# Performance work log

Hardware: AMD Instinct MI355X
Metric: run time of the kernel (lower is better)

Reference implementation:

```python
import jax, jax.numpy as jnp
import numpy as np

N, E, F_IN, NUM_GRAPHS, K = 50000, 500000, 160, 128, 3


def _glorot(k, shape):
    lim = np.sqrt(6.0 / (shape[-2] + shape[-1])).astype(np.float32)
    return jax.random.uniform(k, shape, jnp.float32, -lim, lim)


def setup_inputs() -> dict:
    key = jax.random.key(0)
    ks = jax.random.split(key, 8)
    x = jax.random.normal(ks[0], (N, F_IN), jnp.float32)
    edge_index = jax.random.randint(ks[1], (2, E), 0, N)
    edge_attr = jax.random.uniform(ks[2], (E,), jnp.float32)
    batch = jnp.sort(jax.random.randint(ks[3], (N,), 0, NUM_GRAPHS))
    W1 = _glorot(ks[4], (K, F_IN, 128)); b1 = jnp.zeros((128,), jnp.float32)
    W2 = _glorot(ks[5], (K, 128, 64)); b2 = jnp.zeros((64,), jnp.float32)
    W3 = _glorot(ks[6], (K, 64, 32)); b3 = jnp.zeros((32,), jnp.float32)
    Wl = _glorot(ks[7], (32, 2)); bl = jnp.zeros((2,), jnp.float32)
    return dict(x=x, edge_index=edge_index, edge_attr=edge_attr, batch=batch,
                W1=W1, b1=b1, W2=W2, b2=b2, W3=W3, b3=b3, Wl=Wl, bl=bl)


def _cheb_norm(src, dst, edge_attr, n):
    # PyG ChebConv: sym-normalized Laplacian, lambda_max=2 =>
    # L_hat = (2/lmax)*L_sym - I = -D^{-1/2} A D^{-1/2} (diagonal = 0)
    deg = jax.ops.segment_sum(edge_attr, src, num_segments=n)
    safe = jnp.where(deg > 0, deg, 1.0)
    dinv = jnp.where(deg > 0, jax.lax.rsqrt(safe), 0.0)
    return -dinv[src] * edge_attr * dinv[dst]


def _propagate(x, src, dst, w, n):
    # out[dst] += w * x[src]  (sparse L_hat @ x)
    return jax.ops.segment_sum(w[:, None] * x[src], dst, num_segments=n)


def _cheb_conv(x, src, dst, w, W, b, n):
    # Chebyshev recurrence: T0 = x, T1 = L_hat x, Tk = 2 L_hat T(k-1) - T(k-2)
    tx0 = x
    out = tx0 @ W[0]
    tx1 = _propagate(tx0, src, dst, w, n)
    out = out + tx1 @ W[1]
    for k in range(2, W.shape[0]):
        tx2 = 2.0 * _propagate(tx1, src, dst, w, n) - tx0
        out = out + tx2 @ W[k]
        tx0, tx1 = tx1, tx2
    return out + b


def reference(x, edge_index, edge_attr, batch, W1, b1, W2, b2, W3, b3, Wl, bl):
    n = x.shape[0]
    src, dst = edge_index[0], edge_index[1]
    w = _cheb_norm(src, dst, edge_attr, n)
    h = jax.nn.relu(_cheb_conv(x, src, dst, w, W1, b1, n))
    h = jax.nn.relu(_cheb_conv(h, src, dst, w, W2, b2, n))
    h = jax.nn.relu(_cheb_conv(h, src, dst, w, W3, b3, n))
    # global_mean_pool over graph ids (dropout omitted: eval mode)
    sums = jax.ops.segment_sum(h, batch, num_segments=NUM_GRAPHS)
    cnt = jax.ops.segment_sum(jnp.ones((n,), h.dtype), batch, num_segments=NUM_GRAPHS)
    pooled = sums / jnp.maximum(cnt, 1.0)[:, None]
    return pooled @ Wl + bl
```

## Files before the change

kernel.cpp:

```cpp
#include <hip/hip_runtime.h>

#define N_NODES 50000
#define N_EDGES 500000
#define NUM_G   128
#define SCAN_NB 49
#define PN      (SCAN_NB * 1024)
#define NCX     64
#define ECH     7813
#define RNG     8192
#define NRY     7
#define HVB     (2 * NCX * NRY)
#define CONVB   7813
#define WPREPB  360

typedef __attribute__((ext_vector_type(8))) short short8;
typedef __attribute__((ext_vector_type(4))) float f32x4;

__device__ __forceinline__ unsigned f2bf(float x) {
    unsigned u = __float_as_uint(x);
    return (u + 0x7FFFu + ((u >> 16) & 1u)) >> 16;
}
__device__ __forceinline__ float bf2f(unsigned h) {
    return __uint_as_float(h << 16);
}

__device__ __forceinline__ void wprep_one(const float* __restrict__ W, unsigned short* __restrict__ WT,
                                          int t, int FIN, int F) {
    int n = t / FIN, k = t - n * FIN;
    int sel = n / F, c = n - sel * F;
    float v;
    if (sel == 0) v = W[(size_t)k * F + c] - W[(size_t)2 * FIN * F + (size_t)k * F + c];
    else          v = W[(size_t)sel * FIN * F + (size_t)k * F + c];
    WT[t] = (unsigned short)f2bf(v);
}

__global__ __launch_bounds__(256)
void prep_kernel(const int* __restrict__ src, const int* __restrict__ dst,
                 const float* __restrict__ ea,
                 float* __restrict__ pdeg, int* __restrict__ pcnt,
                 const float* __restrict__ x, unsigned short* __restrict__ Xb,
                 const float* __restrict__ W1, const float* __restrict__ W2,
                 const float* __restrict__ W3,
                 unsigned short* __restrict__ WT1, unsigned short* __restrict__ WT2,
                 unsigned short* __restrict__ WT3) {
    __shared__ unsigned lh[RNG];
    int vb = blockIdx.x, tid = threadIdx.x;
    if (vb < HVB) {
        bool isdeg = vb < NCX * NRY;
        int v2 = isdeg ? vb : vb - NCX * NRY;
        int xk = v2 & 63, y = v2 >> 6;
        int base = y * RNG;
        for (int i = tid; i < RNG; i += 256) lh[i] = 0u;
        __syncthreads();
        int e0 = xk * ECH, e1 = min(e0 + ECH, N_EDGES);
        if (isdeg) {
            for (int e = e0 + tid; e < e1; e += 256) {
                int s = src[e];
                if ((unsigned)(s - base) < RNG) atomicAdd((float*)&lh[s - base], ea[e]);
            }
        } else {
            for (int e = e0 + tid; e < e1; e += 256) {
                int d = dst[e];
                if ((unsigned)(d - base) < RNG) atomicAdd((int*)&lh[d - base], 1);
            }
        }
        __syncthreads();
        if (isdeg) {
            for (int i = tid; i < RNG; i += 256) {
                int n = base + i;
                if (n < PN) pdeg[(size_t)xk * PN + n] = ((float*)lh)[i];
            }
        } else {
            for (int i = tid; i < RNG; i += 256) {
                int n = base + i;
                if (n < PN) pcnt[(size_t)xk * PN + n] = ((int*)lh)[i];
            }
        }
    } else if (vb < HVB + CONVB) {
        int t = (vb - HVB) * 256 + tid;
        if (t < N_NODES * 160 / 4) {
            float4 v = reinterpret_cast<const float4*>(x)[t];
            ushort4 r;
            r.x = (unsigned short)f2bf(v.x);
            r.y = (unsigned short)f2bf(v.y);
            r.z = (unsigned short)f2bf(v.z);
            r.w = (unsigned short)f2bf(v.w);
            *reinterpret_cast<ushort4*>(Xb + (size_t)t * 4) = r;
        }
    } else {
        int t = (vb - HVB - CONVB) * 256 + tid;
        if (t < 61440)      wprep_one(W1, WT1, t, 160, 128);
        else if (t < 86016) wprep_one(W2, WT2, t - 61440, 128, 64);
        else if (t < 92160) wprep_one(W3, WT3, t - 86016, 64, 32);
    }
}

__global__ __launch_bounds__(256)
void reduce_scan_kernel(const float* __restrict__ pdeg, int* __restrict__ pcnt,
                        float* __restrict__ dinv, int* __restrict__ cnt,
                        int* __restrict__ partial) {
    int b = blockIdx.x, t = threadIdx.x;
    int i0 = b * 1024 + t * 4;
    float d0 = 0.f, d1 = 0.f, d2 = 0.f, d3 = 0.f;
    int r0 = 0, r1 = 0, r2 = 0, r3 = 0;
    for (int x = 0; x < NCX; ++x) {
        float4 pv = *reinterpret_cast<const float4*>(pdeg + (size_t)x * PN + i0);
        int4   cv = *reinterpret_cast<const int4*>(pcnt + (size_t)x * PN + i0);
        *reinterpret_cast<int4*>(pcnt + (size_t)x * PN + i0) = make_int4(r0, r1, r2, r3);
        d0 += pv.x; d1 += pv.y; d2 += pv.z; d3 += pv.w;
        r0 += cv.x; r1 += cv.y; r2 += cv.z; r3 += cv.w;
    }
    float dd[4] = {d0, d1, d2, d3};
    int   rr[4] = {r0, r1, r2, r3};
    int s = 0;
    #pragma unroll
    for (int j = 0; j < 4; ++j) {
        int n = i0 + j;
        if (n < N_NODES) {
            float dv = dd[j], r = 0.f;
            if (dv > 0.f) {
                r = rsqrtf(dv);
                r = r * (1.5f - 0.5f * dv * r * r);
            }
            dinv[n] = r;
            cnt[n] = rr[j];
            s += rr[j];
        } else {
            cnt[n] = 0;
        }
    }
    __shared__ int red[256];
    red[t] = s;
    __syncthreads();
    for (int off = 128; off > 0; off >>= 1) {
        if (t < off) red[t] += red[t + off];
        __syncthreads();
    }
    if (t == 0) partial[b] = red[0];
}

__global__ void scan_offsets_kernel(int* __restrict__ partial, int* __restrict__ rowptr,
                                    int nb, int n) {
    int t = threadIdx.x;
    int orig = (t < nb) ? partial[t] : 0;
    int v = orig;
    for (int off = 1; off < 64; off <<= 1) {
        int u = __shfl_up(v, off, 64);
        if (t >= off) v += u;
    }
    if (t < nb) partial[t] = v - orig;
    if (t == nb - 1) rowptr[n] = v;
}

__global__ void scan_final_kernel(const int* __restrict__ cnt, const int* __restrict__ partial,
                                  int* __restrict__ rowptr, int n) {
    int b = blockIdx.x, t = threadIdx.x;
    int4 v = reinterpret_cast<const int4*>(cnt)[b * 256 + t];
    int s = v.x + v.y + v.z + v.w;
    __shared__ int red[256];
    red[t] = s;
    __syncthreads();
    for (int off = 1; off < 256; off <<= 1) {
        int u = (t >= off) ? red[t - off] : 0;
        __syncthreads();
        red[t] += u;
        __syncthreads();
    }
    int excl = partial[b] + ((t == 0) ? 0 : red[t - 1]);
    int i0 = b * 1024 + t * 4;
    if (i0 < n)     rowptr[i0]     = excl;
    if (i0 + 1 < n) rowptr[i0 + 1] = excl + v.x;
    if (i0 + 2 < n) rowptr[i0 + 2] = excl + v.x + v.y;
    if (i0 + 3 < n) rowptr[i0 + 3] = excl + v.x + v.y + v.z;
}

__global__ __launch_bounds__(256)
void scatter_kernel(const int* __restrict__ src, const int* __restrict__ dst,
                    const float* __restrict__ ea,
                    const int* __restrict__ rowptr, const int* __restrict__ pcnt,
                    int2* __restrict__ csr) {
    __shared__ int cursor[RNG];
    int x = blockIdx.x, y = blockIdx.y, tid = threadIdx.x;
    int base = y * RNG;
    for (int i = tid; i < RNG; i += 256) {
        int n = base + i;
        cursor[i] = (n < N_NODES) ? (rowptr[n] + pcnt[(size_t)x * PN + n]) : 0;
    }
    __syncthreads();
    int e0 = x * ECH, e1 = min(e0 + ECH, N_EDGES);
    for (int e = e0 + tid; e < e1; e += 256) {
        int d = dst[e];
        if ((unsigned)(d - base) < RNG) {
            int pos = atomicAdd(&cursor[d - base], 1);
            int2 ew;
            ew.x = src[e];
            ew.y = __float_as_int(ea[e]);
            csr[pos] = ew;
        }
    }
}

template<int FIN, int F>
__launch_bounds__(256)
__global__ void cheb_gemm(const unsigned short* __restrict__ Xb, const unsigned short* __restrict__ WT,
                          const float* __restrict__ dinv,
                          unsigned short* __restrict__ Y0, unsigned short* __restrict__ Y1,
                          unsigned short* __restrict__ Y2,
                          int nrows) {
    constexpr int KT = FIN / 32;
    constexpr int NT = F / 32;
    constexpr int SA = FIN + 8;
    constexpr int F8 = FIN / 8;
    __shared__ short Bs[32 * SA];

    int tid = threadIdx.x;
    int lane = tid & 63, w = tid >> 6;
    int m0 = blockIdx.x * 64;
    int g = blockIdx.y;
    unsigned short* Ys = (g == 0) ? Y0 : (g == 1) ? Y1 : Y2;

    int colb = lane & 15;
    int q8 = (lane >> 4) << 3;
    int rq = (lane >> 4) << 2;
    int arow = m0 + w * 16 + colb;
    bool rok = arow < nrows;

    short8 afr[KT];
    #pragma unroll
    for (int kt = 0; kt < KT; ++kt) {
        short8 z = {0, 0, 0, 0, 0, 0, 0, 0};
        afr[kt] = rok ? *reinterpret_cast<const short8*>(Xb + (size_t)arow * FIN + (kt << 5) + q8) : z;
    }

    for (int nt = 0; nt < NT; ++nt) {
        int n0 = (g * NT + nt) << 5;
        __syncthreads();
        for (int span = tid; span < 32 * F8; span += 256) {
            int r = span / F8, c8 = (span - r * F8) << 3;
            int pr = (r < 16) ? (r << 1) : (((r - 16) << 1) + 1);
            *reinterpret_cast<uint4*>(&Bs[r * SA + c8]) =
                *reinterpret_cast<const uint4*>(WT + (size_t)(n0 + pr) * FIN + c8);
        }
        __syncthreads();

        f32x4 acc0 = {0.f, 0.f, 0.f, 0.f}, acc1 = acc0;
        #pragma unroll
        for (int kt = 0; kt < KT; ++kt) {
            short8 b0 = *reinterpret_cast<const short8*>(&Bs[colb * SA + (kt << 5) + q8]);
            short8 b1 = *reinterpret_cast<const short8*>(&Bs[(colb + 16) * SA + (kt << 5) + q8]);
            acc0 = __builtin_amdgcn_mfma_f32_16x16x32_bf16(afr[kt], b0, acc0, 0, 0, 0);
            acc1 = __builtin_amdgcn_mfma_f32_16x16x32_bf16(afr[kt], b1, acc1, 0, 0, 0);
        }

        int lc = (nt << 5) + (colb << 1);
        #pragma unroll
        for (int r = 0; r < 4; ++r) {
            int orow = m0 + w * 16 + rq + r;
            if (orow < nrows) {
                float sc = (g == 2) ? dinv[orow] : 1.0f;
                unsigned pack = f2bf(acc0[r] * sc) | (f2bf(acc1[r] * sc) << 16);
                *reinterpret_cast<unsigned*>(Ys + (size_t)orow * F + lc) = pack;
            }
        }
    }
}

__device__ __forceinline__ void acc8(float* acc, uint4 p, float wv) {
    acc[0] += wv * bf2f(p.x & 0xFFFFu);
    acc[1] += wv * __uint_as_float(p.x & 0xFFFF0000u);
    acc[2] += wv * bf2f(p.y & 0xFFFFu);
    acc[3] += wv * __uint_as_float(p.y & 0xFFFF0000u);
    acc[4] += wv * bf2f(p.z & 0xFFFFu);
    acc[5] += wv * __uint_as_float(p.z & 0xFFFF0000u);
    acc[6] += wv * bf2f(p.w & 0xFFFFu);
    acc[7] += wv * __uint_as_float(p.w & 0xFFFF0000u);
}

__device__ __forceinline__ void expand8(uint4 p, float* o) {
    o[0] = bf2f(p.x & 0xFFFFu);
    o[1] = __uint_as_float(p.x & 0xFFFF0000u);
    o[2] = bf2f(p.y & 0xFFFFu);
    o[3] = __uint_as_float(p.y & 0xFFFF0000u);
    o[4] = bf2f(p.z & 0xFFFFu);
    o[5] = __uint_as_float(p.z & 0xFFFF0000u);
    o[6] = bf2f(p.w & 0xFFFFu);
    o[7] = __uint_as_float(p.w & 0xFFFF0000u);
}

template<int F, int MODE>
__launch_bounds__(256)
__global__ void gather_kernel(const unsigned short* __restrict__ X, const int2* __restrict__ csr,
                              const int* __restrict__ rowptr, const float* __restrict__ dinv,
                              const unsigned short* __restrict__ Y, const float* __restrict__ bias,
                              unsigned short* __restrict__ O, int n) {
    constexpr int FQ8 = F >> 3;
    constexpr int DPB = 256 / FQ8;
    constexpr int CAP = 2048;
    __shared__ int2 scsr[CAP];
    __shared__ int srp[DPB + 1];
    int tid = threadIdx.x;
    int db0 = blockIdx.x * DPB;
    if (tid <= DPB) srp[tid] = rowptr[min(db0 + tid, n)];
    __syncthreads();
    int ebeg = srp[0];
    int ecnt = srp[DPB] - ebeg;
    bool staged = ecnt <= CAP;
    if (staged) {
        for (int i = tid; i < ecnt; i += 256)
            scsr[i] = csr[ebeg + i];
    }
    __syncthreads();

    int d = db0 + tid / FQ8;
    if (d >= n) return;
    int f8 = (tid % FQ8) << 3;
    float acc[8] = {0.f, 0.f, 0.f, 0.f, 0.f, 0.f, 0.f, 0.f};

    if (staged) {
        int beg = srp[tid / FQ8] - ebeg, end = srp[tid / FQ8 + 1] - ebeg;
        int i = beg;
        for (; i + 7 < end; i += 8) {
            int2 e0 = scsr[i],     e1 = scsr[i + 1], e2 = scsr[i + 2], e3 = scsr[i + 3];
            int2 e4 = scsr[i + 4], e5 = scsr[i + 5], e6 = scsr[i + 6], e7 = scsr[i + 7];
            uint4 p0 = *reinterpret_cast<const uint4*>(X + (size_t)e0.x * F + f8);
            uint4 p1 = *reinterpret_cast<const uint4*>(X + (size_t)e1.x * F + f8);
            uint4 p2 = *reinterpret_cast<const uint4*>(X + (size_t)e2.x * F + f8);
            uint4 p3 = *reinterpret_cast<const uint4*>(X + (size_t)e3.x * F + f8);
            uint4 p4 = *reinterpret_cast<const uint4*>(X + (size_t)e4.x * F + f8);
            uint4 p5 = *reinterpret_cast<const uint4*>(X + (size_t)e5.x * F + f8);
            uint4 p6 = *reinterpret_cast<const uint4*>(X + (size_t)e6.x * F + f8);
            uint4 p7 = *reinterpret_cast<const uint4*>(X + (size_t)e7.x * F + f8);
            acc8(acc, p0, __int_as_float(e0.y));
            acc8(acc, p1, __int_as_float(e1.y));
            acc8(acc, p2, __int_as_float(e2.y));
            acc8(acc, p3, __int_as_float(e3.y));
            acc8(acc, p4, __int_as_float(e4.y));
            acc8(acc, p5, __int_as_float(e5.y));
            acc8(acc, p6, __int_as_float(e6.y));
            acc8(acc, p7, __int_as_float(e7.y));
        }
        for (; i + 3 < end; i += 4) {
            int2 e0 = scsr[i], e1 = scsr[i + 1], e2 = scsr[i + 2], e3 = scsr[i + 3];
            uint4 p0 = *reinterpret_cast<const uint4*>(X + (size_t)e0.x * F + f8);
            uint4 p1 = *reinterpret_cast<const uint4*>(X + (size_t)e1.x * F + f8);
            uint4 p2 = *reinterpret_cast<const uint4*>(X + (size_t)e2.x * F + f8);
            uint4 p3 = *reinterpret_cast<const uint4*>(X + (size_t)e3.x * F + f8);
            acc8(acc, p0, __int_as_float(e0.y));
            acc8(acc, p1, __int_as_float(e1.y));
            acc8(acc, p2, __int_as_float(e2.y));
            acc8(acc, p3, __int_as_float(e3.y));
        }
        for (; i < end; ++i) {
            int2 e = scsr[i];
            uint4 p = *reinterpret_cast<const uint4*>(X + (size_t)e.x * F + f8);
            acc8(acc, p, __int_as_float(e.y));
        }
    } else {
        int beg = srp[tid / FQ8], end = srp[tid / FQ8 + 1];
        for (int i = beg; i < end; ++i) {
            int2 e = csr[i];
            uint4 p = *reinterpret_cast<const uint4*>(X + (size_t)e.x * F + f8);
            acc8(acc, p, __int_as_float(e.y));
        }
    }

    float y[8];
    expand8(*reinterpret_cast<const uint4*>(Y + (size_t)d * F + f8), y);
    float dv = dinv[d];
    float v[8];
    if (MODE == 0) {
        float dv2 = 2.f * dv;
        #pragma unroll
        for (int j = 0; j < 8; ++j) v[j] = dv * (y[j] - dv2 * acc[j]);
    } else {
        float4 ba = *reinterpret_cast<const float4*>(bias + f8);
        float4 bb = *reinterpret_cast<const float4*>(bias + f8 + 4);
        v[0] = fmaxf(y[0] - dv * acc[0] + ba.x, 0.f);
        v[1] = fmaxf(y[1] - dv * acc[1] + ba.y, 0.f);
        v[2] = fmaxf(y[2] - dv * acc[2] + ba.z, 0.f);
        v[3] = fmaxf(y[3] - dv * acc[3] + ba.w, 0.f);
        v[4] = fmaxf(y[4] - dv * acc[4] + bb.x, 0.f);
        v[5] = fmaxf(y[5] - dv * acc[5] + bb.y, 0.f);
        v[6] = fmaxf(y[6] - dv * acc[6] + bb.z, 0.f);
        v[7] = fmaxf(y[7] - dv * acc[7] + bb.w, 0.f);
    }
    uint4 o;
    o.x = f2bf(v[0]) | (f2bf(v[1]) << 16);
    o.y = f2bf(v[2]) | (f2bf(v[3]) << 16);
    o.z = f2bf(v[4]) | (f2bf(v[5]) << 16);
    o.w = f2bf(v[6]) | (f2bf(v[7]) << 16);
    *reinterpret_cast<uint4*>(O + (size_t)d * F + f8) = o;
}

__device__ __forceinline__ int lower_bound_dev(const int* __restrict__ a, int n, int v) {
    int lo = 0, hi = n;
    while (lo < hi) {
        int mid = (lo + hi) >> 1;
        if (a[mid] < v) lo = mid + 1; else hi = mid;
    }
    return lo;
}

__global__ void pool_kernel(const unsigned short* __restrict__ H, const int* __restrict__ batch,
                            const float* __restrict__ Wl, const float* __restrict__ bl,
                            float* __restrict__ out, int n) {
    int g = blockIdx.x;
    int start = lower_bound_dev(batch, n, g);
    int end   = lower_bound_dev(batch, n, g + 1);
    int tid = threadIdx.x;
    int f = tid & 31;
    int sub = tid >> 5;
    float acc = 0.0f;
    for (int i = start + sub; i < end; i += 8)
        acc += bf2f((unsigned)H[(size_t)i * 32 + f]);
    __shared__ float red[256];
    red[tid] = acc;
    __syncthreads();
    if (tid < 128) red[tid] += red[tid + 128];
    __syncthreads();
    if (tid < 64) red[tid] += red[tid + 64];
    __syncthreads();
    if (tid < 32) red[tid] += red[tid + 32];
    __syncthreads();
    if (tid < 2) {
        int cnt = end - start;
        float inv = 1.0f / (float)(cnt > 0 ? cnt : 1);
        float o = bl[tid];
        for (int f2 = 0; f2 < 32; ++f2)
            o += red[f2] * inv * Wl[f2 * 2 + tid];
        out[g * 2 + tid] = o;
    }
}

extern "C" void kernel_launch(void* const* d_in, const int* in_sizes, int n_in,
                              void* d_out, int out_size, void* d_ws, size_t ws_size,
                              hipStream_t stream) {
    const float* x     = (const float*)d_in[0];
    const int*   ei    = (const int*)d_in[1];
    const float* ea    = (const float*)d_in[2];
    const int*   batch = (const int*)d_in[3];
    const float* W1 = (const float*)d_in[4];
    const float* b1 = (const float*)d_in[5];
    const float* W2 = (const float*)d_in[6];
    const float* b2 = (const float*)d_in[7];
    const float* W3 = (const float*)d_in[8];
    const float* b3 = (const float*)d_in[9];
    const float* Wl = (const float*)d_in[10];
    const float* bl = (const float*)d_in[11];
    float* out = (float*)d_out;
    char* ws = (char*)d_ws;

    const int* src = ei;
    const int* dst = ei + N_EDGES;

    size_t off = 0;
    auto alloc = [&](size_t bytes) { char* p = ws + off; off += (bytes + 255) & ~(size_t)255; return p; };
    float* pdeg    = (float*)alloc((size_t)NCX * PN * 4);
    int*   pcnt    = (int*)  alloc((size_t)NCX * PN * 4);
    float* dinv    = (float*)alloc(N_NODES * 4);
    int*   cnt     = (int*)  alloc((size_t)PN * 4);
    int*   partial = (int*)  alloc(SCAN_NB * 4);
    int*   rowptr  = (int*)  alloc((N_NODES + 1) * 4);
    int2*  csr     = (int2*) alloc((size_t)N_EDGES * 8);
    unsigned short* Xb  = (unsigned short*)alloc((size_t)N_NODES * 160 * 2);
    unsigned short* Y0  = (unsigned short*)alloc((size_t)N_NODES * 128 * 2);
    unsigned short* Y1  = (unsigned short*)alloc((size_t)N_NODES * 128 * 2);
    unsigned short* Y2  = (unsigned short*)alloc((size_t)N_NODES * 128 * 2);
    unsigned short* U   = (unsigned short*)alloc((size_t)N_NODES * 128 * 2);
    unsigned short* WT1 = (unsigned short*)alloc((size_t)384 * 160 * 2);
    unsigned short* WT2 = (unsigned short*)alloc((size_t)192 * 128 * 2);
    unsigned short* WT3 = (unsigned short*)alloc((size_t)96 * 64 * 2);

    const int BT = 256;

    prep_kernel<<<HVB + CONVB + WPREPB, BT, 0, stream>>>(src, dst, ea, pdeg, pcnt,
                                                         x, Xb, W1, W2, W3, WT1, WT2, WT3);
    reduce_scan_kernel<<<SCAN_NB, BT, 0, stream>>>(pdeg, pcnt, dinv, cnt, partial);
    scan_offsets_kernel<<<1, 64, 0, stream>>>(partial, rowptr, SCAN_NB, N_NODES);
    scan_final_kernel<<<SCAN_NB, BT, 0, stream>>>(cnt, partial, rowptr, N_NODES);
    scatter_kernel<<<dim3(NCX, NRY), BT, 0, stream>>>(src, dst, ea, rowptr, pcnt, csr);

    dim3 ggrid((N_NODES + 63) / 64, 3);
    auto gb = [&](int F) { int DPB = 256 / (F / 8); return (N_NODES + DPB - 1) / DPB; };

    cheb_gemm<160, 128><<<ggrid, BT, 0, stream>>>(Xb, WT1, dinv, Y0, Y1, Y2, N_NODES);
    gather_kernel<128, 0><<<gb(128), BT, 0, stream>>>(Y2, csr, rowptr, dinv, Y1, nullptr, U, N_NODES);
    gather_kernel<128, 1><<<gb(128), BT, 0, stream>>>(U, csr, rowptr, dinv, Y0, b1, Xb, N_NODES);

    cheb_gemm<128, 64><<<ggrid, BT, 0, stream>>>(Xb, WT2, dinv, Y0, Y1, Y2, N_NODES);
    gather_kernel<64, 0><<<gb(64), BT, 0, stream>>>(Y2, csr, rowptr, dinv, Y1, nullptr, U, N_NODES);
    gather_kernel<64, 1><<<gb(64), BT, 0, stream>>>(U, csr, rowptr, dinv, Y0, b2, Xb, N_NODES);

    cheb_gemm<64, 32><<<ggrid, BT, 0, stream>>>(Xb, WT3, dinv, Y0, Y1, Y2, N_NODES);
    gather_kernel<32, 0><<<gb(32), BT, 0, stream>>>(Y2, csr, rowptr, dinv, Y1, nullptr, U, N_NODES);
    gather_kernel<32, 1><<<gb(32), BT, 0, stream>>>(U, csr, rowptr, dinv, Y0, b3, Xb, N_NODES);

    pool_kernel<<<NUM_G, BT, 0, stream>>>(Xb, batch, Wl, bl, out, N_NODES);
}
```

Before: 322.3 us.

## Fuse scan offsets into scan_final and co-launch scatter with first GEMM

Folds the single-block scan_offsets kernel into scan_final_kernel, with each block recomputing the 49-entry prefix via wave shuffles. Merges the CSR scatter and the layer-1 Chebyshev GEMM into one launch that dispatches on block index, since they are independent and can overlap. This removes two kernel launches and the serialization between them. In exchange the merged kernel reserves 32KB of shared memory for all blocks, which may reduce occupancy for the GEMM blocks.

```diff
diff --git a/kernel.cpp b/kernel.cpp
--- a/kernel.cpp
+++ b/kernel.cpp
@@ -12,6 +12,8 @@
 #define HVB     (2 * NCX * NRY)
 #define CONVB   7813
 #define WPREPB  360
+#define SCVB    (NCX * NRY)
+#define GEMM_MB 782
 
 typedef __attribute__((ext_vector_type(8))) short short8;
 typedef __attribute__((ext_vector_type(4))) float f32x4;
@@ -139,25 +141,26 @@
     if (t == 0) partial[b] = red[0];
 }
 
-__global__ void scan_offsets_kernel(int* __restrict__ partial, int* __restrict__ rowptr,
-                                    int nb, int n) {
-    int t = threadIdx.x;
-    int orig = (t < nb) ? partial[t] : 0;
-    int v = orig;
-    for (int off = 1; off < 64; off <<= 1) {
-        int u = __shfl_up(v, off, 64);
-        if (t >= off) v += u;
-    }
-    if (t < nb) partial[t] = v - orig;
-    if (t == nb - 1) rowptr[n] = v;
-}
-
-__global__ void scan_final_kernel(const int* __restrict__ cnt, const int* __restrict__ partial,
-                                  int* __restrict__ rowptr, int n) {
+__global__ __launch_bounds__(256)
+void scan_final_kernel(const int* __restrict__ cnt, const int* __restrict__ partial,
+                       int* __restrict__ rowptr, int n) {
     int b = blockIdx.x, t = threadIdx.x;
+    __shared__ int red[256];
+    __shared__ int sh_off, sh_tot;
+    if (t < 64) {
+        int orig = (t < SCAN_NB) ? partial[t] : 0;
+        int v = orig;
+        #pragma unroll
+        for (int off = 1; off < 64; off <<= 1) {
+            int u = __shfl_up(v, off, 64);
+            if (t >= off) v += u;
+        }
+        if (t == b) sh_off = v - orig;
+        if (t == SCAN_NB - 1) sh_tot = v;
+    }
+    __syncthreads();
     int4 v = reinterpret_cast<const int4*>(cnt)[b * 256 + t];
     int s = v.x + v.y + v.z + v.w;
-    __shared__ int red[256];
     red[t] = s;
     __syncthreads();
     for (int off = 1; off < 256; off <<= 1) {
@@ -166,21 +169,22 @@
         red[t] += u;
         __syncthreads();
     }
-    int excl = partial[b] + ((t == 0) ? 0 : red[t - 1]);
+    int excl = sh_off + ((t == 0) ? 0 : red[t - 1]);
     int i0 = b * 1024 + t * 4;
     if (i0 < n)     rowptr[i0]     = excl;
     if (i0 + 1 < n) rowptr[i0 + 1] = excl + v.x;
     if (i0 + 2 < n) rowptr[i0 + 2] = excl + v.x + v.y;
     if (i0 + 3 < n) rowptr[i0 + 3] = excl + v.x + v.y + v.z;
-}
-
-__global__ __launch_bounds__(256)
-void scatter_kernel(const int* __restrict__ src, const int* __restrict__ dst,
-                    const float* __restrict__ ea,
-                    const int* __restrict__ rowptr, const int* __restrict__ pcnt,
-                    int2* __restrict__ csr) {
-    __shared__ int cursor[RNG];
-    int x = blockIdx.x, y = blockIdx.y, tid = threadIdx.x;
+    if (b == SCAN_NB - 1 && t == 0) rowptr[n] = sh_tot;
+}
+
+__device__ void scatter_body(int vb, const int* __restrict__ src, const int* __restrict__ dst,
+                             const float* __restrict__ ea,
+                             const int* __restrict__ rowptr, const int* __restrict__ pcnt,
+                             int2* __restrict__ csr, unsigned char* smraw) {
+    int* cursor = (int*)smraw;
+    int tid = threadIdx.x;
+    int x = vb & 63, y = vb >> 6;
     int base = y * RNG;
     for (int i = tid; i < RNG; i += 256) {
         int n = base + i;
@@ -201,22 +205,19 @@
 }
 
 template<int FIN, int F>
-__launch_bounds__(256)
-__global__ void cheb_gemm(const unsigned short* __restrict__ Xb, const unsigned short* __restrict__ WT,
-                          const float* __restrict__ dinv,
+__device__ void gemm_body(int bx, int g, const unsigned short* __restrict__ Xb,
+                          const unsigned short* __restrict__ WT, const float* __restrict__ dinv,
                           unsigned short* __restrict__ Y0, unsigned short* __restrict__ Y1,
-                          unsigned short* __restrict__ Y2,
-                          int nrows) {
+                          unsigned short* __restrict__ Y2, int nrows, unsigned char* smraw) {
     constexpr int KT = FIN / 32;
     constexpr int NT = F / 32;
     constexpr int SA = FIN + 8;
     constexpr int F8 = FIN / 8;
-    __shared__ short Bs[32 * SA];
+    short* Bs = (short*)smraw;
 
     int tid = threadIdx.x;
     int lane = tid & 63, w = tid >> 6;
-    int m0 = blockIdx.x * 64;
-    int g = blockIdx.y;
+    int m0 = bx * 64;
     unsigned short* Ys = (g == 0) ? Y0 : (g == 1) ? Y1 : Y2;
 
     int colb = lane & 15;
@@ -263,6 +264,35 @@
             }
         }
     }
+}
+
+__global__ __launch_bounds__(256)
+void sg_kernel(const int* __restrict__ src, const int* __restrict__ dst,
+               const float* __restrict__ ea,
+               const int* __restrict__ rowptr, const int* __restrict__ pcnt,
+               int2* __restrict__ csr,
+               const unsigned short* __restrict__ Xb, const unsigned short* __restrict__ WT1,
+               const float* __restrict__ dinv,
+               unsigned short* __restrict__ Y0, unsigned short* __restrict__ Y1,
+               unsigned short* __restrict__ Y2) {
+    __shared__ alignas(16) unsigned char sm[32768];
+    int vb = blockIdx.x;
+    if (vb < SCVB) {
+        scatter_body(vb, src, dst, ea, rowptr, pcnt, csr, sm);
+    } else {
+        int v2 = vb - SCVB;
+        gemm_body<160, 128>(v2 % GEMM_MB, v2 / GEMM_MB, Xb, WT1, dinv, Y0, Y1, Y2, N_NODES, sm);
+    }
+}
+
+template<int FIN, int F>
+__launch_bounds__(256)
+__global__ void cheb_gemm(const unsigned short* __restrict__ Xb, const unsigned short* __restrict__ WT,
+                          const float* __restrict__ dinv,
+                          unsigned short* __restrict__ Y0, unsigned short* __restrict__ Y1,
+                          unsigned short* __restrict__ Y2, int nrows) {
+    __shared__ alignas(16) unsigned char sm[32 * (FIN + 8) * 2];
+    gemm_body<FIN, F>(blockIdx.x, blockIdx.y, Xb, WT, dinv, Y0, Y1, Y2, nrows, sm);
 }
 
 __device__ __forceinline__ void acc8(float* acc, uint4 p, float wv) {
@@ -476,14 +506,13 @@
     prep_kernel<<<HVB + CONVB + WPREPB, BT, 0, stream>>>(src, dst, ea, pdeg, pcnt,
                                                          x, Xb, W1, W2, W3, WT1, WT2, WT3);
     reduce_scan_kernel<<<SCAN_NB, BT, 0, stream>>>(pdeg, pcnt, dinv, cnt, partial);
-    scan_offsets_kernel<<<1, 64, 0, stream>>>(partial, rowptr, SCAN_NB, N_NODES);
     scan_final_kernel<<<SCAN_NB, BT, 0, stream>>>(cnt, partial, rowptr, N_NODES);
-    scatter_kernel<<<dim3(NCX, NRY), BT, 0, stream>>>(src, dst, ea, rowptr, pcnt, csr);
-
-    dim3 ggrid((N_NODES + 63) / 64, 3);
+    sg_kernel<<<SCVB + 3 * GEMM_MB, BT, 0, stream>>>(src, dst, ea, rowptr, pcnt, csr,
+                                                     Xb, WT1, dinv, Y0, Y1, Y2);
+
+    dim3 ggrid(GEMM_MB, 3);
     auto gb = [&](int F) { int DPB = 256 / (F / 8); return (N_NODES + DPB - 1) / DPB; };
 
-    cheb_gemm<160, 128><<<ggrid, BT, 0, stream>>>(Xb, WT1, dinv, Y0, Y1, Y2, N_NODES);
     gather_kernel<128, 0><<<gb(128), BT, 0, stream>>>(Y2, csr, rowptr, dinv, Y1, nullptr, U, N_NODES);
     gather_kernel<128, 1><<<gb(128), BT, 0, stream>>>(U, csr, rowptr, dinv, Y0, b1, Xb, N_NODES);
 
```

After: 312.0 us, median of 2. 1.03x faster.
